# Optimization experiments

Measured on AMD Instinct MI355X. Metric: run time of the kernel, lower is better.

The kernel has to match this reference:

```python
import jax, jax.numpy as jnp
import numpy as np
import math

SQRT15 = math.sqrt(15.0)

def _commutator(X, Y):
    # [X, Y] = XY - YX, batched over leading dims
    return X @ Y - Y @ X

def setup_inputs() -> dict:
    key = jax.random.key(0)
    kA, ky = jax.random.split(key)
    B, d = 131072, 8
    A = jax.random.normal(kA, (B, 3, d, d), dtype=jnp.float32) * 0.1
    h = jnp.asarray(0.01, dtype=jnp.float32)
    y0 = jax.random.normal(ky, (B, d), dtype=jnp.float32)
    return {"A": A, "h": h, "y0": y0}

def reference(A, h, y0):
    # A: [B, 3, d, d] matrices at the three Gauss-Legendre nodes; h: scalar; y0: [B, d]
    A1, A2, A3 = A[:, 0], A[:, 1], A[:, 2]
    alpha1 = h * A2
    alpha2 = h * (SQRT15 / 3.0) * (A3 - A1)
    alpha3 = h * (10.0 / 3.0) * (A1 - 2.0 * A2 + A3)
    C1 = _commutator(alpha1, alpha2)
    C2 = (-1.0 / 60.0) * _commutator(alpha1, 2.0 * alpha3 + C1)
    term_in_comm = -20.0 * alpha1 - alpha3 + C1
    term_with_comm = alpha2 + C2
    Omega = alpha1 + alpha3 / 12.0 + (1.0 / 240.0) * _commutator(term_in_comm, term_with_comm)
    U = jax.vmap(jax.scipy.linalg.expm)(Omega)  # batched matrix exponential
    y_next = jnp.einsum('bij,bj->bi', U, y0)
    return y_next
```

## Files before the change

### kernel.cpp

```cpp
#include <hip/hip_runtime.h>

#define NT 256


typedef float v2f __attribute__((ext_vector_type(2)));

template <int O>
__device__ __forceinline__ float qb(float x) {
    return __int_as_float(__builtin_amdgcn_mov_dpp(
        __float_as_int(x), O * 0x55, 0xF, 0xF, true));
}
template <int O>
__device__ __forceinline__ v2f qb2(v2f y) {
    v2f r;
    r.x = qb<O>(y.x);
    r.y = qb<O>(y.y);
    return r;
}
__device__ __forceinline__ v2f pkfma(v2f a, v2f b, v2f c) {
    return __builtin_elementwise_fma(a, b, c);
}

template <int SGN, int O>
__device__ __forceinline__ void mm4_o(v2f (&acc)[8], const v2f (&X)[8],
                                      const v2f (&Y)[8]) {
#pragma unroll
    for (int s = 0; s < 2; ++s) {
        v2f w2[4];
#pragma unroll
        for (int jj = 0; jj < 4; ++jj) w2[jj] = qb2<O>(Y[s * 4 + jj]);
#pragma unroll
        for (int r = 0; r < 2; ++r) {
            const float x0 = (s == 0) ? X[r * 4 + O].x : X[r * 4 + O].y;
            const float xs = (SGN > 0) ? x0 : -x0;
            const v2f xx = {xs, xs};
#pragma unroll
            for (int jj = 0; jj < 4; ++jj)
                acc[r * 4 + jj] = pkfma(xx, w2[jj], acc[r * 4 + jj]);
        }
    }
}

template <int SGN>
__device__ __forceinline__ void mm4(v2f (&acc)[8], const v2f (&X)[8],
                                    const v2f (&Y)[8]) {
    mm4_o<SGN, 0>(acc, X, Y);
    mm4_o<SGN, 1>(acc, X, Y);
    mm4_o<SGN, 2>(acc, X, Y);
    mm4_o<SGN, 3>(acc, X, Y);
}

__global__ __launch_bounds__(NT)
void magnus6_kernel(const float* __restrict__ A,
                    const float* __restrict__ hp,
                    const float* __restrict__ y0,
                    float* __restrict__ out,
                    int B)
{
    __shared__ float4 lds[4][NT];

    const int tx = threadIdx.x;
    const int t  = blockIdx.x * NT + tx;
    const int p  = t >> 2;
    const int q  = t & 3;
    if (p >= B) return;

    const float h    = hp[0];
    const float c_a2 = h * 1.2909944487358056f;
    const float c_a3 = h * (10.0f / 3.0f);
    const float c_m  = 20.0f / 3.0f;

    const float4* __restrict__ Ap =
        reinterpret_cast<const float4*>(A + (size_t)p * 192 + q * 16);

    v2f R1[8];
    v2f R2[8];
    v2f R3[8];

#pragma unroll
    for (int c = 0; c < 4; ++c) {
        float4 v1 = Ap[c], v2 = Ap[16 + c], v3 = Ap[32 + c];
        const int b = (c >> 1) * 4 + (c & 1) * 2;
        v2f A1lo = {v1.x, v1.y}, A1hi = {v1.z, v1.w};
        v2f A2lo = {v2.x, v2.y}, A2hi = {v2.z, v2.w};
        v2f A3lo = {v3.x, v3.y}, A3hi = {v3.z, v3.w};
        v2f al1lo = h * A2lo, al1hi = h * A2hi;
        R1[b] = al1lo; R1[b + 1] = al1hi;
        R2[b]     = c_a2 * (A3lo - A1lo);
        R2[b + 1] = c_a2 * (A3hi - A1hi);
        v2f a3lo = c_a3 * (A1lo + A3lo) - c_m * al1lo;
        v2f a3hi = c_a3 * (A1hi + A3hi) - c_m * al1hi;
        lds[c][tx] = make_float4(a3lo.x, a3lo.y, a3hi.x, a3hi.y);
    }

#pragma unroll
    for (int i = 0; i < 8; ++i) R3[i] = (v2f){0.0f, 0.0f};
    mm4<+1>(R3, R1, R2);
    mm4<-1>(R3, R2, R1);

#pragma unroll
    for (int c = 0; c < 4; ++c) {
        float4 v = lds[c][tx];
        v2f a3lo = {v.x, v.y}, a3hi = {v.z, v.w};
        const int b = (c >> 1) * 4 + (c & 1) * 2;
        const v2f k60 = {1.0f / 60.0f, 1.0f / 60.0f};
        R3[b]     = pkfma(R3[b],     k60, (1.0f / 30.0f) * a3lo);
        R3[b + 1] = pkfma(R3[b + 1], k60, (1.0f / 30.0f) * a3hi);
    }

    mm4<-1>(R2, R1, R3);
    mm4<+1>(R2, R3, R1);

#pragma unroll
    for (int c = 0; c < 4; ++c) {
        float4 v = lds[c][tx];
        v2f a3lo = {v.x, v.y}, a3hi = {v.z, v.w};
        const int b = (c >> 1) * 4 + (c & 1) * 2;
        v2f t0 = R3[b], t1 = R3[b + 1];
        v2f a10 = R1[b], a11 = R1[b + 1];
        R3[b]     = 0.25f * t0 - (1.0f / 12.0f) * a10 - (1.0f / 80.0f) * a3lo;
        R3[b + 1] = 0.25f * t1 - (1.0f / 12.0f) * a11 - (1.0f / 80.0f) * a3hi;
        R1[b]     = a10 + (1.0f / 12.0f) * a3lo;
        R1[b + 1] = a11 + (1.0f / 12.0f) * a3hi;
    }

    mm4<+1>(R1, R3, R2);
    mm4<-1>(R1, R2, R3);

    const float2 y0v = *reinterpret_cast<const float2*>(y0 + (size_t)p * 8 + 2 * q);
    float v0 = y0v.x, v1 = y0v.y;
    float yy0 = v0, yy1 = v1;

    const float inv[6] = {1.0f, 0.5f, 1.0f / 3.0f, 0.25f, 0.2f, 1.0f / 6.0f};
#pragma unroll
    for (int k = 0; k < 6; ++k) {
        v2f acc0 = {0.0f, 0.0f}, acc1 = {0.0f, 0.0f};
        {
            v2f vw;
            vw.x = qb<0>(v0); vw.y = qb<0>(v1);
            acc0 = pkfma(R1[0], vw, acc0); acc1 = pkfma(R1[4], vw, acc1);
            vw.x = qb<1>(v0); vw.y = qb<1>(v1);
            acc0 = pkfma(R1[1], vw, acc0); acc1 = pkfma(R1[5], vw, acc1);
            vw.x = qb<2>(v0); vw.y = qb<2>(v1);
            acc0 = pkfma(R1[2], vw, acc0); acc1 = pkfma(R1[6], vw, acc1);
            vw.x = qb<3>(v0); vw.y = qb<3>(v1);
            acc0 = pkfma(R1[3], vw, acc0); acc1 = pkfma(R1[7], vw, acc1);
        }
        v0 = (acc0.x + acc0.y) * inv[k];
        v1 = (acc1.x + acc1.y) * inv[k];
        yy0 += v0;
        yy1 += v1;
    }

    *reinterpret_cast<float2*>(out + (size_t)p * 8 + 2 * q) = make_float2(yy0, yy1);
}

extern "C" void kernel_launch(void* const* d_in, const int* in_sizes, int n_in,
                              void* d_out, int out_size, void* d_ws, size_t ws_size,
                              hipStream_t stream)
{
    const float* A  = (const float*)d_in[0];
    const float* hp = (const float*)d_in[1];
    const float* y0 = (const float*)d_in[2];
    float* out = (float*)d_out;

    const int B = in_sizes[2] / 8;
    const int nthreads = 4 * B;
    const int grid = (nthreads + NT - 1) / NT;
    magnus6_kernel<<<grid, NT, 0, stream>>>(A, hp, y0, out, B);
}
```

Measured before the change: 24.70 us.

## Redistribute 8x8 matrix tiles across 4 lanes as 2x2 blocks with new DPP shuffles

```diff
diff --git a/kernel.cpp b/kernel.cpp
--- a/kernel.cpp
+++ b/kernel.cpp
@@ -5,49 +5,50 @@
 
 typedef float v2f __attribute__((ext_vector_type(2)));
 
-template <int O>
-__device__ __forceinline__ float qb(float x) {
+template <int CTRL>
+__device__ __forceinline__ float qbp(float x) {
     return __int_as_float(__builtin_amdgcn_mov_dpp(
-        __float_as_int(x), O * 0x55, 0xF, 0xF, true));
-}
-template <int O>
-__device__ __forceinline__ v2f qb2(v2f y) {
-    v2f r;
-    r.x = qb<O>(y.x);
-    r.y = qb<O>(y.y);
-    return r;
+        __float_as_int(x), CTRL, 0xF, 0xF, true));
 }
 __device__ __forceinline__ v2f pkfma(v2f a, v2f b, v2f c) {
     return __builtin_elementwise_fma(a, b, c);
 }
 
-template <int SGN, int O>
-__device__ __forceinline__ void mm4_o(v2f (&acc)[8], const v2f (&X)[8],
-                                      const v2f (&Y)[8]) {
+template <int SGN, int K>
+__device__ __forceinline__ void mmk(v2f (&acc)[8], const v2f (&X)[8],
+                                    const v2f (&Y)[8]) {
+    constexpr int XPAT = (K >> 2) ? 0xF5 : 0xA0;
+    constexpr int YPAT = (K & 1) ? 0xEE : 0x44;
+    constexpr int XPI  = (K & 3) >> 1;
+    float xs[4];
 #pragma unroll
-    for (int s = 0; s < 2; ++s) {
-        v2f w2[4];
+    for (int lr = 0; lr < 4; ++lr) {
+        const float s = (K & 1) ? X[lr * 2 + XPI].y : X[lr * 2 + XPI].x;
+        xs[lr] = qbp<XPAT>(s);
+    }
+    v2f yv[2];
 #pragma unroll
-        for (int jj = 0; jj < 4; ++jj) w2[jj] = qb2<O>(Y[s * 4 + jj]);
+    for (int lc = 0; lc < 2; ++lc) {
+        yv[lc].x = qbp<YPAT>(Y[(K >> 1) * 2 + lc].x);
+        yv[lc].y = qbp<YPAT>(Y[(K >> 1) * 2 + lc].y);
+    }
 #pragma unroll
-        for (int r = 0; r < 2; ++r) {
-            const float x0 = (s == 0) ? X[r * 4 + O].x : X[r * 4 + O].y;
-            const float xs = (SGN > 0) ? x0 : -x0;
-            const v2f xx = {xs, xs};
+    for (int lr = 0; lr < 4; ++lr) {
+        const float m = SGN > 0 ? xs[lr] : -xs[lr];
+        const v2f xx = {m, m};
 #pragma unroll
-            for (int jj = 0; jj < 4; ++jj)
-                acc[r * 4 + jj] = pkfma(xx, w2[jj], acc[r * 4 + jj]);
-        }
+        for (int lc = 0; lc < 2; ++lc)
+            acc[lr * 2 + lc] = pkfma(xx, yv[lc], acc[lr * 2 + lc]);
     }
 }
 
 template <int SGN>
 __device__ __forceinline__ void mm4(v2f (&acc)[8], const v2f (&X)[8],
                                     const v2f (&Y)[8]) {
-    mm4_o<SGN, 0>(acc, X, Y);
-    mm4_o<SGN, 1>(acc, X, Y);
-    mm4_o<SGN, 2>(acc, X, Y);
-    mm4_o<SGN, 3>(acc, X, Y);
+    mmk<SGN, 0>(acc, X, Y); mmk<SGN, 1>(acc, X, Y);
+    mmk<SGN, 2>(acc, X, Y); mmk<SGN, 3>(acc, X, Y);
+    mmk<SGN, 4>(acc, X, Y); mmk<SGN, 5>(acc, X, Y);
+    mmk<SGN, 6>(acc, X, Y); mmk<SGN, 7>(acc, X, Y);
 }
 
 __global__ __launch_bounds__(NT)
@@ -64,6 +65,10 @@
     const int p  = t >> 2;
     const int q  = t & 3;
     if (p >= B) return;
+    const int r0 = q >> 1;
+    const int ch = q & 1;
+    const bool oddrow = (r0 != 0);
+    const bool hihalf = (ch != 0);
 
     const float h    = hp[0];
     const float c_a2 = h * 1.2909944487358056f;
@@ -71,26 +76,27 @@
     const float c_m  = 20.0f / 3.0f;
 
     const float4* __restrict__ Ap =
-        reinterpret_cast<const float4*>(A + (size_t)p * 192 + q * 16);
+        reinterpret_cast<const float4*>(A) + (size_t)p * 48 + q;
 
     v2f R1[8];
     v2f R2[8];
     v2f R3[8];
 
 #pragma unroll
-    for (int c = 0; c < 4; ++c) {
-        float4 v1 = Ap[c], v2 = Ap[16 + c], v3 = Ap[32 + c];
-        const int b = (c >> 1) * 4 + (c & 1) * 2;
-        v2f A1lo = {v1.x, v1.y}, A1hi = {v1.z, v1.w};
-        v2f A2lo = {v2.x, v2.y}, A2hi = {v2.z, v2.w};
-        v2f A3lo = {v3.x, v3.y}, A3hi = {v3.z, v3.w};
+    for (int i = 0; i < 4; ++i) {
+        float4 f1 = Ap[4 * i];
+        float4 f2 = Ap[16 + 4 * i];
+        float4 f3 = Ap[32 + 4 * i];
+        v2f A1lo = {f1.x, f1.y}, A1hi = {f1.z, f1.w};
+        v2f A2lo = {f2.x, f2.y}, A2hi = {f2.z, f2.w};
+        v2f A3lo = {f3.x, f3.y}, A3hi = {f3.z, f3.w};
         v2f al1lo = h * A2lo, al1hi = h * A2hi;
-        R1[b] = al1lo; R1[b + 1] = al1hi;
-        R2[b]     = c_a2 * (A3lo - A1lo);
-        R2[b + 1] = c_a2 * (A3hi - A1hi);
+        R1[2 * i] = al1lo; R1[2 * i + 1] = al1hi;
+        R2[2 * i]     = c_a2 * (A3lo - A1lo);
+        R2[2 * i + 1] = c_a2 * (A3hi - A1hi);
         v2f a3lo = c_a3 * (A1lo + A3lo) - c_m * al1lo;
         v2f a3hi = c_a3 * (A1hi + A3hi) - c_m * al1hi;
-        lds[c][tx] = make_float4(a3lo.x, a3lo.y, a3hi.x, a3hi.y);
+        lds[i][tx] = make_float4(a3lo.x, a3lo.y, a3hi.x, a3hi.y);
     }
 
 #pragma unroll
@@ -102,10 +108,9 @@
     for (int c = 0; c < 4; ++c) {
         float4 v = lds[c][tx];
         v2f a3lo = {v.x, v.y}, a3hi = {v.z, v.w};
-        const int b = (c >> 1) * 4 + (c & 1) * 2;
         const v2f k60 = {1.0f / 60.0f, 1.0f / 60.0f};
-        R3[b]     = pkfma(R3[b],     k60, (1.0f / 30.0f) * a3lo);
-        R3[b + 1] = pkfma(R3[b + 1], k60, (1.0f / 30.0f) * a3hi);
+        R3[2 * c]     = pkfma(R3[2 * c],     k60, (1.0f / 30.0f) * a3lo);
+        R3[2 * c + 1] = pkfma(R3[2 * c + 1], k60, (1.0f / 30.0f) * a3hi);
     }
 
     mm4<-1>(R2, R1, R3);
@@ -115,44 +120,62 @@
     for (int c = 0; c < 4; ++c) {
         float4 v = lds[c][tx];
         v2f a3lo = {v.x, v.y}, a3hi = {v.z, v.w};
-        const int b = (c >> 1) * 4 + (c & 1) * 2;
-        v2f t0 = R3[b], t1 = R3[b + 1];
-        v2f a10 = R1[b], a11 = R1[b + 1];
-        R3[b]     = 0.25f * t0 - (1.0f / 12.0f) * a10 - (1.0f / 80.0f) * a3lo;
-        R3[b + 1] = 0.25f * t1 - (1.0f / 12.0f) * a11 - (1.0f / 80.0f) * a3hi;
-        R1[b]     = a10 + (1.0f / 12.0f) * a3lo;
-        R1[b + 1] = a11 + (1.0f / 12.0f) * a3hi;
+        v2f t0 = R3[2 * c], t1 = R3[2 * c + 1];
+        v2f a10 = R1[2 * c], a11 = R1[2 * c + 1];
+        R3[2 * c]     = 0.25f * t0 - (1.0f / 12.0f) * a10 - (1.0f / 80.0f) * a3lo;
+        R3[2 * c + 1] = 0.25f * t1 - (1.0f / 12.0f) * a11 - (1.0f / 80.0f) * a3hi;
+        R1[2 * c]     = a10 + (1.0f / 12.0f) * a3lo;
+        R1[2 * c + 1] = a11 + (1.0f / 12.0f) * a3hi;
     }
 
     mm4<+1>(R1, R3, R2);
     mm4<-1>(R1, R2, R3);
 
-    const float2 y0v = *reinterpret_cast<const float2*>(y0 + (size_t)p * 8 + 2 * q);
-    float v0 = y0v.x, v1 = y0v.y;
-    float yy0 = v0, yy1 = v1;
+    const float4 vh4 =
+        reinterpret_cast<const float4*>(y0 + (size_t)p * 8)[ch];
+    v2f vh[2] = {{vh4.x, vh4.y}, {vh4.z, vh4.w}};
+
+    float isel0 = oddrow ? vh[0].y : vh[0].x;
+    float isel1 = oddrow ? vh[1].y : vh[1].x;
+    float ya[4];
+    ya[0] = qbp<0xA0>(isel0);
+    ya[1] = qbp<0xA0>(isel1);
+    ya[2] = qbp<0xF5>(isel0);
+    ya[3] = qbp<0xF5>(isel1);
 
     const float inv[6] = {1.0f, 0.5f, 1.0f / 3.0f, 0.25f, 0.2f, 1.0f / 6.0f};
+    float vn[4];
 #pragma unroll
     for (int k = 0; k < 6; ++k) {
-        v2f acc0 = {0.0f, 0.0f}, acc1 = {0.0f, 0.0f};
-        {
-            v2f vw;
-            vw.x = qb<0>(v0); vw.y = qb<0>(v1);
-            acc0 = pkfma(R1[0], vw, acc0); acc1 = pkfma(R1[4], vw, acc1);
-            vw.x = qb<1>(v0); vw.y = qb<1>(v1);
-            acc0 = pkfma(R1[1], vw, acc0); acc1 = pkfma(R1[5], vw, acc1);
-            vw.x = qb<2>(v0); vw.y = qb<2>(v1);
-            acc0 = pkfma(R1[2], vw, acc0); acc1 = pkfma(R1[6], vw, acc1);
-            vw.x = qb<3>(v0); vw.y = qb<3>(v1);
-            acc0 = pkfma(R1[3], vw, acc0); acc1 = pkfma(R1[7], vw, acc1);
+        float w[4];
+#pragma unroll
+        for (int lr = 0; lr < 4; ++lr) {
+            v2f pv = pkfma(R1[lr * 2 + 1], vh[1], R1[lr * 2] * vh[0]);
+            const float ph = pv.x + pv.y;
+            w[lr] = ph + qbp<0xB1>(ph);
         }
-        v0 = (acc0.x + acc0.y) * inv[k];
-        v1 = (acc1.x + acc1.y) * inv[k];
-        yy0 += v0;
-        yy1 += v1;
+#pragma unroll
+        for (int lr = 0; lr < 4; ++lr) {
+            vn[lr] = w[lr] * inv[k];
+            ya[lr] += vn[lr];
+        }
+        if (k < 5) {
+            const float s0 = hihalf ? vn[2] : vn[0];
+            const float s1 = hihalf ? vn[3] : vn[1];
+            vh[0].x = qbp<0x44>(s0);
+            vh[0].y = qbp<0xEE>(s0);
+            vh[1].x = qbp<0x44>(s1);
+            vh[1].y = qbp<0xEE>(s1);
+        }
     }
 
-    *reinterpret_cast<float2*>(out + (size_t)p * 8 + 2 * q) = make_float2(yy0, yy1);
+    if (ch == 0) {
+        float* ob = out + (size_t)p * 8 + r0;
+        ob[0] = ya[0];
+        ob[2] = ya[1];
+        ob[4] = ya[2];
+        ob[6] = ya[3];
+    }
 }
 
 extern "C" void kernel_launch(void* const* d_in, const int* in_sizes, int n_in,
```

After: 26.70 us. +8.1%, slower.

## Persistent grid with async global-to-LDS prefetch of next matrix batch

Applied to the files above, without the earlier changes.

```diff
diff --git a/kernel.cpp b/kernel.cpp
--- a/kernel.cpp
+++ b/kernel.cpp
@@ -1,6 +1,8 @@
 #include <hip/hip_runtime.h>
 
-#define NT 256
+#define NT   256
+#define NBLK 512
+#define PPI  (NBLK * NT / 4)
 
 
 typedef float v2f __attribute__((ext_vector_type(2)));
@@ -40,7 +42,6 @@
         }
     }
 }
-
 template <int SGN>
 __device__ __forceinline__ void mm4(v2f (&acc)[8], const v2f (&X)[8],
                                     const v2f (&Y)[8]) {
@@ -50,92 +51,133 @@
     mm4_o<SGN, 3>(acc, X, Y);
 }
 
+__device__ __forceinline__ void glds1(const float4* g, float4* l) {
+    __builtin_amdgcn_global_load_lds(
+        (const __attribute__((address_space(1))) void*)g,
+        (__attribute__((address_space(3))) void*)l,
+        16, 0, 0);
+}
+
+__device__ __forceinline__ void stage_all(const float4* g, float4* l) {
+    glds1(g + 0,  l + 0 * 64);   glds1(g + 1,  l + 1 * 64);
+    glds1(g + 2,  l + 2 * 64);   glds1(g + 3,  l + 3 * 64);
+    glds1(g + 16, l + 4 * 64);   glds1(g + 17, l + 5 * 64);
+    glds1(g + 18, l + 6 * 64);   glds1(g + 19, l + 7 * 64);
+    glds1(g + 32, l + 8 * 64);   glds1(g + 33, l + 9 * 64);
+    glds1(g + 34, l + 10 * 64);  glds1(g + 35, l + 11 * 64);
+}
+
 __global__ __launch_bounds__(NT)
 void magnus6_kernel(const float* __restrict__ A,
                     const float* __restrict__ hp,
                     const float* __restrict__ y0,
                     float* __restrict__ out,
-                    int B)
+                    int B, int NI)
 {
-    __shared__ float4 lds[4][NT];
-
-    const int tx = threadIdx.x;
-    const int t  = blockIdx.x * NT + tx;
-    const int p  = t >> 2;
-    const int q  = t & 3;
-    if (p >= B) return;
+    __shared__ float4 stage[4][12][64];
+    __shared__ float4 a3s[4][NT];
+
+    const int tx    = threadIdx.x;
+    const int w     = tx >> 6;
+    const int lane  = tx & 63;
+    const int q     = tx & 3;
+    const int pslot = blockIdx.x * (NT / 4) + (tx >> 2);
 
     const float h    = hp[0];
     const float c_a2 = h * 1.2909944487358056f;
     const float c_a3 = h * (10.0f / 3.0f);
     const float c_m  = 20.0f / 3.0f;
 
-    const float4* __restrict__ Ap =
-        reinterpret_cast<const float4*>(A + (size_t)p * 192 + q * 16);
-
-    v2f R1[8];
-    v2f R2[8];
-    v2f R3[8];
-
-#pragma unroll
-    for (int c = 0; c < 4; ++c) {
-        float4 v1 = Ap[c], v2 = Ap[16 + c], v3 = Ap[32 + c];
-        const int b = (c >> 1) * 4 + (c & 1) * 2;
-        v2f A1lo = {v1.x, v1.y}, A1hi = {v1.z, v1.w};
-        v2f A2lo = {v2.x, v2.y}, A2hi = {v2.z, v2.w};
-        v2f A3lo = {v3.x, v3.y}, A3hi = {v3.z, v3.w};
-        v2f al1lo = h * A2lo, al1hi = h * A2hi;
-        R1[b] = al1lo; R1[b + 1] = al1hi;
-        R2[b]     = c_a2 * (A3lo - A1lo);
-        R2[b + 1] = c_a2 * (A3hi - A1hi);
-        v2f a3lo = c_a3 * (A1lo + A3lo) - c_m * al1lo;
-        v2f a3hi = c_a3 * (A1hi + A3hi) - c_m * al1hi;
-        lds[c][tx] = make_float4(a3lo.x, a3lo.y, a3hi.x, a3hi.y);
+    const float4* __restrict__ A4 = reinterpret_cast<const float4*>(A);
+    float4* sb = &stage[w][0][0];
+
+    {
+        const int pn = pslot;
+        const int pc = pn < B ? pn : B - 1;
+        stage_all(A4 + (size_t)pc * 48 + q * 4, sb);
     }
 
-#pragma unroll
-    for (int i = 0; i < 8; ++i) R3[i] = (v2f){0.0f, 0.0f};
-    mm4<+1>(R3, R1, R2);
-    mm4<-1>(R3, R2, R1);
-
-#pragma unroll
-    for (int c = 0; c < 4; ++c) {
-        float4 v = lds[c][tx];
-        v2f a3lo = {v.x, v.y}, a3hi = {v.z, v.w};
-        const int b = (c >> 1) * 4 + (c & 1) * 2;
-        const v2f k60 = {1.0f / 60.0f, 1.0f / 60.0f};
-        R3[b]     = pkfma(R3[b],     k60, (1.0f / 30.0f) * a3lo);
-        R3[b + 1] = pkfma(R3[b + 1], k60, (1.0f / 30.0f) * a3hi);
-    }
-
-    mm4<-1>(R2, R1, R3);
-    mm4<+1>(R2, R3, R1);
-
-#pragma unroll
-    for (int c = 0; c < 4; ++c) {
-        float4 v = lds[c][tx];
-        v2f a3lo = {v.x, v.y}, a3hi = {v.z, v.w};
-        const int b = (c >> 1) * 4 + (c & 1) * 2;
-        v2f t0 = R3[b], t1 = R3[b + 1];
-        v2f a10 = R1[b], a11 = R1[b + 1];
-        R3[b]     = 0.25f * t0 - (1.0f / 12.0f) * a10 - (1.0f / 80.0f) * a3lo;
-        R3[b + 1] = 0.25f * t1 - (1.0f / 12.0f) * a11 - (1.0f / 80.0f) * a3hi;
-        R1[b]     = a10 + (1.0f / 12.0f) * a3lo;
-        R1[b + 1] = a11 + (1.0f / 12.0f) * a3hi;
-    }
-
-    mm4<+1>(R1, R3, R2);
-    mm4<-1>(R1, R2, R3);
-
-    const float2 y0v = *reinterpret_cast<const float2*>(y0 + (size_t)p * 8 + 2 * q);
-    float v0 = y0v.x, v1 = y0v.y;
-    float yy0 = v0, yy1 = v1;
-
-    const float inv[6] = {1.0f, 0.5f, 1.0f / 3.0f, 0.25f, 0.2f, 1.0f / 6.0f};
-#pragma unroll
-    for (int k = 0; k < 6; ++k) {
-        v2f acc0 = {0.0f, 0.0f}, acc1 = {0.0f, 0.0f};
-        {
+    for (int n = 0; n < NI; ++n) {
+        const int p   = n * PPI + pslot;
+        const int pcl = p < B ? p : B - 1;
+
+        asm volatile("s_waitcnt vmcnt(0)" ::: "memory");
+        __builtin_amdgcn_sched_barrier(0);
+
+        const float2 y0v =
+            *reinterpret_cast<const float2*>(y0 + (size_t)pcl * 8 + 2 * q);
+
+        v2f R1[8];
+        v2f R2[8];
+        v2f R3[8];
+
+#pragma unroll
+        for (int c = 0; c < 4; ++c) {
+            float4 v1 = stage[w][c][lane];
+            float4 v2 = stage[w][4 + c][lane];
+            float4 v3 = stage[w][8 + c][lane];
+            const int b = (c >> 1) * 4 + (c & 1) * 2;
+            v2f A1lo = {v1.x, v1.y}, A1hi = {v1.z, v1.w};
+            v2f A2lo = {v2.x, v2.y}, A2hi = {v2.z, v2.w};
+            v2f A3lo = {v3.x, v3.y}, A3hi = {v3.z, v3.w};
+            v2f al1lo = h * A2lo, al1hi = h * A2hi;
+            R1[b] = al1lo; R1[b + 1] = al1hi;
+            R2[b]     = c_a2 * (A3lo - A1lo);
+            R2[b + 1] = c_a2 * (A3hi - A1hi);
+            v2f a3lo = c_a3 * (A1lo + A3lo) - c_m * al1lo;
+            v2f a3hi = c_a3 * (A1hi + A3hi) - c_m * al1hi;
+            a3s[c][tx] = make_float4(a3lo.x, a3lo.y, a3hi.x, a3hi.y);
+        }
+
+        asm volatile("s_waitcnt lgkmcnt(0)" ::: "memory");
+        __builtin_amdgcn_sched_barrier(0);
+        if (n + 1 < NI) {
+            const int pn = (n + 1) * PPI + pslot;
+            const int pc = pn < B ? pn : B - 1;
+            stage_all(A4 + (size_t)pc * 48 + q * 4, sb);
+        }
+        __builtin_amdgcn_sched_barrier(0);
+
+#pragma unroll
+        for (int i = 0; i < 8; ++i) R3[i] = (v2f){0.0f, 0.0f};
+        mm4<+1>(R3, R1, R2);
+        mm4<-1>(R3, R2, R1);
+
+#pragma unroll
+        for (int c = 0; c < 4; ++c) {
+            float4 v = a3s[c][tx];
+            v2f a3lo = {v.x, v.y}, a3hi = {v.z, v.w};
+            const int b = (c >> 1) * 4 + (c & 1) * 2;
+            const v2f k60 = {1.0f / 60.0f, 1.0f / 60.0f};
+            R3[b]     = pkfma(R3[b],     k60, (1.0f / 30.0f) * a3lo);
+            R3[b + 1] = pkfma(R3[b + 1], k60, (1.0f / 30.0f) * a3hi);
+        }
+
+        mm4<-1>(R2, R1, R3);
+        mm4<+1>(R2, R3, R1);
+
+#pragma unroll
+        for (int c = 0; c < 4; ++c) {
+            float4 v = a3s[c][tx];
+            v2f a3lo = {v.x, v.y}, a3hi = {v.z, v.w};
+            const int b = (c >> 1) * 4 + (c & 1) * 2;
+            v2f t0 = R3[b], t1 = R3[b + 1];
+            v2f a10 = R1[b], a11 = R1[b + 1];
+            R3[b]     = 0.25f * t0 - (1.0f / 12.0f) * a10 - (1.0f / 80.0f) * a3lo;
+            R3[b + 1] = 0.25f * t1 - (1.0f / 12.0f) * a11 - (1.0f / 80.0f) * a3hi;
+            R1[b]     = a10 + (1.0f / 12.0f) * a3lo;
+            R1[b + 1] = a11 + (1.0f / 12.0f) * a3hi;
+        }
+
+        mm4<+1>(R1, R3, R2);
+        mm4<-1>(R1, R2, R3);
+
+        float v0 = y0v.x, v1 = y0v.y;
+        float yy0 = v0, yy1 = v1;
+        const float inv[6] = {1.0f, 0.5f, 1.0f / 3.0f, 0.25f, 0.2f, 1.0f / 6.0f};
+#pragma unroll
+        for (int k = 0; k < 6; ++k) {
+            v2f acc0 = {0.0f, 0.0f}, acc1 = {0.0f, 0.0f};
             v2f vw;
             vw.x = qb<0>(v0); vw.y = qb<0>(v1);
             acc0 = pkfma(R1[0], vw, acc0); acc1 = pkfma(R1[4], vw, acc1);
@@ -145,14 +187,16 @@
             acc0 = pkfma(R1[2], vw, acc0); acc1 = pkfma(R1[6], vw, acc1);
             vw.x = qb<3>(v0); vw.y = qb<3>(v1);
             acc0 = pkfma(R1[3], vw, acc0); acc1 = pkfma(R1[7], vw, acc1);
-        }
-        v0 = (acc0.x + acc0.y) * inv[k];
-        v1 = (acc1.x + acc1.y) * inv[k];
-        yy0 += v0;
-        yy1 += v1;
+            v0 = (acc0.x + acc0.y) * inv[k];
+            v1 = (acc1.x + acc1.y) * inv[k];
+            yy0 += v0;
+            yy1 += v1;
+        }
+
+        if (p < B)
+            *reinterpret_cast<float2*>(out + (size_t)p * 8 + 2 * q) =
+                make_float2(yy0, yy1);
     }
-
-    *reinterpret_cast<float2*>(out + (size_t)p * 8 + 2 * q) = make_float2(yy0, yy1);
 }
 
 extern "C" void kernel_launch(void* const* d_in, const int* in_sizes, int n_in,
@@ -164,8 +208,7 @@
     const float* y0 = (const float*)d_in[2];
     float* out = (float*)d_out;
 
-    const int B = in_sizes[2] / 8;
-    const int nthreads = 4 * B;
-    const int grid = (nthreads + NT - 1) / NT;
-    magnus6_kernel<<<grid, NT, 0, stream>>>(A, hp, y0, out, B);
-}
+    const int B  = in_sizes[2] / 8;
+    const int NI = (B + PPI - 1) / PPI;
+    magnus6_kernel<<<NBLK, NT, 0, stream>>>(A, hp, y0, out, B, NI);
+}
```

Result: slower. 29.13 us (+17.9%).
